# Kernel tuning notes

Hardware: AMD Instinct MI355X
Metric: run time of the kernel (lower is better)

Reference implementation:

```python
import jax, jax.numpy as jnp
import numpy as np

B, S, D = 2, 2048, 2048
NH = 16
HD = D // NH  # 128
MAX_POS = 4096
ROPE_THETA = 10000.0


def rotate_half(x):
    x1, x2 = x[..., : x.shape[-1] // 2], x[..., x.shape[-1] // 2 :]
    return jnp.concatenate((-x2, x1), axis=-1)


def rope_tables(dtype=jnp.float32):
    inv_freq = 1.0 / (ROPE_THETA ** (jnp.arange(0, HD, 2, dtype=jnp.float32) / HD))
    t = jnp.arange(MAX_POS, dtype=jnp.float32)
    freqs = jnp.outer(t, inv_freq)              # [MAX_POS, HD/2]
    emb = jnp.concatenate((freqs, freqs), axis=-1)  # [MAX_POS, HD]
    return jnp.cos(emb).astype(dtype), jnp.sin(emb).astype(dtype)


def setup_inputs() -> dict:
    key = jax.random.key(0)
    ks = jax.random.split(key, 9)
    sc = 0.02
    return {
        "hidden_states": jax.random.normal(ks[0], (B, S, D), jnp.float32),
        "position_ids": jnp.arange(B * S, dtype=jnp.int32).reshape(B, S),
        "Wq": jax.random.normal(ks[1], (D, D), jnp.float32) * sc,
        "bq": jax.random.normal(ks[2], (D,), jnp.float32) * sc,
        "Wk": jax.random.normal(ks[3], (D, D), jnp.float32) * sc,
        "bk": jax.random.normal(ks[4], (D,), jnp.float32) * sc,
        "Wv": jax.random.normal(ks[5], (D, D), jnp.float32) * sc,
        "bv": jax.random.normal(ks[6], (D,), jnp.float32) * sc,
        "Wo": jax.random.normal(ks[7], (D, D), jnp.float32) * sc,
    }


def reference(hidden_states, position_ids, Wq, bq, Wk, bk, Wv, bv, Wo):
    b, s, _ = hidden_states.shape
    # projections (torch Linear: x @ W.T + b)
    q = (hidden_states @ Wq.T + bq).reshape(b, s, NH, HD).transpose(0, 2, 1, 3)
    k = (hidden_states @ Wk.T + bk).reshape(b, s, NH, HD).transpose(0, 2, 1, 3)
    v = (hidden_states @ Wv.T + bv).reshape(b, s, NH, HD).transpose(0, 2, 1, 3)
    # RoPE
    cos_t, sin_t = rope_tables(hidden_states.dtype)
    cos = cos_t[position_ids][:, None, :, :]  # [B,1,S,HD]
    sin = sin_t[position_ids][:, None, :, :]
    q = q * cos + rotate_half(q) * sin
    k = k * cos + rotate_half(k) * sin
    # NOTE: faithful to the source bug — softmax is computed but its result is
    # discarded; the AV matmul uses the UNNORMALIZED scaled scores.
    attn_weights = jnp.einsum("bhqd,bhkd->bhqk", q, k) / (HD ** 0.5)
    _ = jax.nn.softmax(attn_weights.astype(jnp.float32), axis=-1)  # dead, as in source
    attn_output = jnp.einsum("bhqk,bhkd->bhqd", attn_weights, v)
    attn_output = attn_output.transpose(0, 2, 1, 3).reshape(b, s, D)
    return attn_output @ Wo.T
```

## Files before the change

kernel.cpp:

```cpp
#include <hip/hip_runtime.h>
#include <hip/hip_bf16.h>


typedef __attribute__((ext_vector_type(8))) short bf16x8s;
typedef __attribute__((ext_vector_type(4))) float f32x4;

__device__ __forceinline__ ushort f2bf(float f) {
    union { float f; unsigned int u; } x; x.f = f;
    unsigned int u = x.u;
    unsigned int r = (u + 0x7fffu + ((u >> 16) & 1u)) >> 16;
    return (ushort)r;
}
__device__ __forceinline__ float b2f(ushort u) {
    union { unsigned int u; float f; } x; x.u = ((unsigned int)u) << 16;
    return x.f;
}

__device__ __forceinline__ void gload_lds16(const void* g, void* l) {
    __builtin_amdgcn_global_load_lds((__attribute__((address_space(1))) const void*)g,
                                     (__attribute__((address_space(3))) void*)l, 16, 0, 0);
}

template<bool BIAS, bool OBF16>
__global__ __launch_bounds__(512, 2)
void gemm256(const ushort* __restrict__ A, const ushort* __restrict__ B,
             const float* __restrict__ bias, void* __restrict__ Cv,
             int K, int lda, int ldb, int ldc,
             long sAb, long sBb, long sCb)
{
    __shared__ char smem[131072];
    char* ldsA = smem;
    char* ldsB = smem + 65536;

    int z = blockIdx.z;
    const ushort* Ab = A + (size_t)sAb * z;
    const ushort* Bb = B + (size_t)sBb * z;
    size_t Coff = (size_t)sCb * z;

    int nwgx = gridDim.x;
    int nwg = nwgx * gridDim.y;
    int wg = blockIdx.y * nwgx + blockIdx.x;
    int swz = ((nwg & 7) == 0) ? (wg & 7) * (nwg >> 3) + (wg >> 3) : wg;
    int m0 = (swz % nwgx) * 256;
    int n0 = (swz / nwgx) * 256;

    int tid = threadIdx.x;
    int l = tid & 63, wid = tid >> 6;
    int wm = (wid >> 2) * 128;
    int wn = (wid & 3) * 64;
    int lr = l & 15, lj = l >> 4;

    int offA[8], offB[4];
#pragma unroll
    for (int m = 0; m < 8; m++) {
        int r = wm + m * 16 + lr;
        offA[m] = (r >> 1) * 128 + (((((r & 1) << 2) | lj) ^ ((r >> 1) & 7)) << 4);
    }
#pragma unroll
    for (int n = 0; n < 4; n++) {
        int r = wn + n * 16 + lr;
        offB[n] = (r >> 1) * 128 + (((((r & 1) << 2) | lj) ^ ((r >> 1) & 7)) << 4);
    }

    size_t srcA[2], srcB[2];
    int dstOff[2];
#pragma unroll
    for (int s = 0; s < 2; s++) {
        int c = tid + s * 512;
        int pr = c >> 3;
        int up = (c & 7) ^ (pr & 7);
        int r = (pr << 1) | (up >> 2);
        int jj = up & 3;
        srcA[s] = (size_t)(m0 + r) * lda + jj * 8;
        srcB[s] = (size_t)(n0 + r) * ldb + jj * 8;
        dstOff[s] = c * 16;
    }

    f32x4 acc[8][4];
#pragma unroll
    for (int m = 0; m < 8; m++)
#pragma unroll
        for (int n = 0; n < 4; n++)
            acc[m][n] = (f32x4){0.f, 0.f, 0.f, 0.f};

    int NT2 = K >> 5;

#define STAGE256(T) { int _bo = ((T) & 3) * 16384; size_t _ko = (size_t)(T) * 32; \
    gload_lds16(Ab + srcA[0] + _ko, ldsA + _bo + dstOff[0]); \
    gload_lds16(Ab + srcA[1] + _ko, ldsA + _bo + dstOff[1]); \
    gload_lds16(Bb + srcB[0] + _ko, ldsB + _bo + dstOff[0]); \
    gload_lds16(Bb + srcB[1] + _ko, ldsB + _bo + dstOff[1]); }

    STAGE256(0);
    STAGE256(1);
    asm volatile("s_waitcnt vmcnt(4)" ::: "memory");
    __builtin_amdgcn_s_barrier();

    for (int t = 0; t < NT2; ++t) {
        if (t + 2 < NT2) {
            STAGE256(t + 2);
            __builtin_amdgcn_sched_barrier(0);
        }
        int bo = (t & 3) * 16384;
        bf16x8s bf[4];
#pragma unroll
        for (int n = 0; n < 4; n++)
            bf[n] = *(const bf16x8s*)(ldsB + bo + offB[n]);
        bf16x8s af[8];
#pragma unroll
        for (int m = 0; m < 8; m++)
            af[m] = *(const bf16x8s*)(ldsA + bo + offA[m]);
#pragma unroll
        for (int m = 0; m < 8; m++)
#pragma unroll
            for (int n = 0; n < 4; n++)
                acc[m][n] = __builtin_amdgcn_mfma_f32_16x16x32_bf16(
                    af[m], bf[n], acc[m][n], 0, 0, 0);
        if (t + 1 < NT2) {
            if (t + 2 < NT2) asm volatile("s_waitcnt vmcnt(4)" ::: "memory");
            else             asm volatile("s_waitcnt vmcnt(0)" ::: "memory");
            __builtin_amdgcn_s_barrier();
        }
    }
#undef STAGE256

    int rr = lj * 4;
#pragma unroll
    for (int m = 0; m < 8; m++) {
#pragma unroll
        for (int n = 0; n < 4; n++) {
            int gr = m0 + wm + m * 16 + rr;
            int gc = n0 + wn + n * 16 + lr;
            float bv = BIAS ? bias[gc] : 0.f;
#pragma unroll
            for (int r = 0; r < 4; r++) {
                float v = acc[m][n][r] + bv;
                size_t off = Coff + (size_t)(gr + r) * ldc + gc;
                if (OBF16) ((ushort*)Cv)[off] = f2bf(v);
                else       ((float*)Cv)[off]  = v;
            }
        }
    }
}

template<bool BIAS, bool OBF16, int BN>
__global__ __launch_bounds__(256)
void gemm_nt(const ushort* __restrict__ A, const ushort* __restrict__ B,
             const float* __restrict__ bias, void* __restrict__ Cv,
             int K, int lda, int ldb, int ldc, int ZH,
             long sAb, long sAh, long sBb, long sBh, long sCb, long sCh)
{
    __shared__ ushort As[128 * 32];
    __shared__ ushort Bs[BN * 32];

    int z  = blockIdx.z;
    int zb = z / ZH, zh = z - zb * ZH;
    const ushort* Ab = A + (size_t)(sAb * zb + sAh * zh);
    const ushort* Bb = B + (size_t)(sBb * zb + sBh * zh);
    size_t Coff = (size_t)(sCb * zb + sCh * zh);

    int m0 = blockIdx.x * 128, n0 = blockIdx.y * BN;
    int t = threadIdx.x;
    int l = t & 63, w = t >> 6;
    int wm, wn;
    if (BN == 128) { wm = (w >> 1) * 64; wn = (w & 1) * 64; }
    else           { wm = w * 32;        wn = 0; }
    constexpr int FM = (BN == 128) ? 4 : 2;
    constexpr int FN = 4;
    int lr = l & 15, lk = (l >> 4) * 8;

    f32x4 acc[FM][FN];
#pragma unroll
    for (int i = 0; i < FM; i++)
#pragma unroll
        for (int j = 0; j < FN; j++)
            acc[i][j] = (f32x4){0.f, 0.f, 0.f, 0.f};

    int c0 = t, c1 = t + 256;
    int r0 = c0 >> 2, k0c = (c0 & 3) * 8;
    int r1 = c1 >> 2, k1c = (c1 & 3) * 8;

    for (int kt = 0; kt < K; kt += 32) {
        __syncthreads();
        gload_lds16(Ab + (size_t)(m0 + r0) * lda + kt + k0c, &As[c0 * 8]);
        gload_lds16(Ab + (size_t)(m0 + r1) * lda + kt + k1c, &As[c1 * 8]);
        gload_lds16(Bb + (size_t)(n0 + r0) * ldb + kt + k0c, &Bs[c0 * 8]);
        if (BN == 128)
            gload_lds16(Bb + (size_t)(n0 + r1) * ldb + kt + k1c, &Bs[c1 * 8]);
        __syncthreads();

        bf16x8s af[FM], bf[FN];
#pragma unroll
        for (int i = 0; i < FM; i++)
            af[i] = *(const bf16x8s*)&As[(wm + i * 16 + lr) * 32 + lk];
#pragma unroll
        for (int i = 0; i < FN; i++)
            bf[i] = *(const bf16x8s*)&Bs[(wn + i * 16 + lr) * 32 + lk];
#pragma unroll
        for (int mi = 0; mi < FM; mi++)
#pragma unroll
            for (int ni = 0; ni < FN; ni++)
                acc[mi][ni] = __builtin_amdgcn_mfma_f32_16x16x32_bf16(
                    af[mi], bf[ni], acc[mi][ni], 0, 0, 0);
    }

    int rr = (l >> 4) * 4;
#pragma unroll
    for (int mi = 0; mi < FM; mi++) {
#pragma unroll
        for (int ni = 0; ni < FN; ni++) {
            int gr = m0 + wm + mi * 16 + rr;
            int gc = n0 + wn + ni * 16 + lr;
            float bv = BIAS ? bias[gc] : 0.f;
#pragma unroll
            for (int r = 0; r < 4; r++) {
                float v = acc[mi][ni][r] + bv;
                size_t off = Coff + (size_t)(gr + r) * ldc + gc;
                if (OBF16) ((ushort*)Cv)[off] = f2bf(v);
                else       ((float*)Cv)[off]  = v;
            }
        }
    }
}

__global__ __launch_bounds__(256)
void rope_qk(ushort* __restrict__ QKV, const int* __restrict__ pos,
             ushort* __restrict__ QB)
{
    int tid = blockIdx.x * 256 + threadIdx.x;
    int row = tid >> 7;
    int r = tid & 127;
    int h = r >> 3, j = r & 7;
    int d0 = j * 8;
    float p = (float)pos[row];
    size_t qb = (size_t)row * 6144 + h * 128 + d0;

    bf16x8s q1 = *(const bf16x8s*)&QKV[qb];
    bf16x8s q2 = *(const bf16x8s*)&QKV[qb + 64];
    bf16x8s k1 = *(const bf16x8s*)&QKV[qb + 2048];
    bf16x8s k2 = *(const bf16x8s*)&QKV[qb + 2048 + 64];
    bf16x8s oq1, oq2, ok1, ok2;
#pragma unroll
    for (int i = 0; i < 8; i++) {
        float d = (float)(d0 + i);
        float ang = p * exp2f(d * (-13.287712379549449f / 64.0f));
        float s, c;
        sincosf(ang, &s, &c);
        float a = b2f((ushort)q1[i]), b = b2f((ushort)q2[i]);
        oq1[i] = (short)f2bf(a * c - b * s);
        oq2[i] = (short)f2bf(b * c + a * s);
        float e = b2f((ushort)k1[i]), f = b2f((ushort)k2[i]);
        ok1[i] = (short)f2bf(e * c - f * s);
        ok2[i] = (short)f2bf(f * c + e * s);
    }
    size_t ob = (size_t)row * 2048 + h * 128 + d0;
    *(bf16x8s*)&QB[ob]      = oq1;
    *(bf16x8s*)&QB[ob + 64] = oq2;
    *(bf16x8s*)&QKV[qb + 2048]      = ok1;
    *(bf16x8s*)&QKV[qb + 2048 + 64] = ok2;
}

__global__ __launch_bounds__(256)
void ktv_partial(const ushort* __restrict__ QKV, float* __restrict__ part)
{
    int bh = blockIdx.x;
    int b = bh >> 4, h = bh & 15;
    int s0 = blockIdx.y * 128;
    const ushort* Kp = QKV + (size_t)(b * 2048 + s0) * 6144 + 2048 + h * 128;
    const ushort* Vp = Kp + 2048;

    __shared__ ushort Ks[32][128];
    __shared__ ushort Vs[32][128];

    int t = threadIdx.x;
    int tx = t & 15, ty = t >> 4;
    float acc[8][8];
#pragma unroll
    for (int i = 0; i < 8; i++)
#pragma unroll
        for (int j = 0; j < 8; j++) acc[i][j] = 0.f;

    for (int sb = 0; sb < 128; sb += 32) {
        __syncthreads();
#pragma unroll
        for (int i = 0; i < 2; i++) {
            int idx = t + i * 256;
            int rw = idx >> 4, c8 = (idx & 15) * 8;
            *(bf16x8s*)&Ks[rw][c8] = *(const bf16x8s*)&Kp[(size_t)(sb + rw) * 6144 + c8];
            *(bf16x8s*)&Vs[rw][c8] = *(const bf16x8s*)&Vp[(size_t)(sb + rw) * 6144 + c8];
        }
        __syncthreads();
        for (int ss = 0; ss < 32; ss++) {
            bf16x8s kvv = *(const bf16x8s*)&Ks[ss][tx * 8];
            bf16x8s vvv = *(const bf16x8s*)&Vs[ss][ty * 8];
            float kv[8], vv[8];
#pragma unroll
            for (int i = 0; i < 8; i++) { kv[i] = b2f((ushort)kvv[i]); vv[i] = b2f((ushort)vvv[i]); }
#pragma unroll
            for (int i = 0; i < 8; i++)
#pragma unroll
                for (int j = 0; j < 8; j++)
                    acc[i][j] += kv[i] * vv[j];
        }
    }
    float* pp = part + ((size_t)blockIdx.y * 32 + bh) * 16384;
#pragma unroll
    for (int i = 0; i < 8; i++)
#pragma unroll
        for (int j = 0; j < 8; j++)
            pp[(tx * 8 + i) * 128 + (ty * 8 + j)] = acc[i][j];
}

__global__ __launch_bounds__(256)
void reduce_ktv(const float* __restrict__ part, ushort* __restrict__ Mb)
{
    int i = blockIdx.x * 256 + threadIdx.x;
    float s = 0.f;
#pragma unroll
    for (int p = 0; p < 16; p++) s += part[(size_t)p * 524288 + i];
    Mb[i] = f2bf(s * 0.08838834764831845f);
}

__global__ __launch_bounds__(256)
void conv_f32_bf16(const float* __restrict__ in, ushort* __restrict__ out, int n4)
{
    int i = blockIdx.x * 256 + threadIdx.x;
    if (i >= n4) return;
    float4 v = ((const float4*)in)[i];
    ushort4 o;
    o.x = f2bf(v.x); o.y = f2bf(v.y); o.z = f2bf(v.z); o.w = f2bf(v.w);
    ((ushort4*)out)[i] = o;
}

__global__ __launch_bounds__(256)
void conv_weights(const float* __restrict__ w0, const float* __restrict__ w1,
                  const float* __restrict__ w2, const float* __restrict__ w3,
                  ushort* __restrict__ qkv, ushort* __restrict__ wo)
{
    int i = blockIdx.x * 256 + threadIdx.x;
    int id = i >> 20;
    int off = i & 1048575;
    const float* src = (id == 0) ? w0 : (id == 1) ? w1 : (id == 2) ? w2 : w3;
    float4 v = ((const float4*)src)[off];
    ushort4 o;
    o.x = f2bf(v.x); o.y = f2bf(v.y); o.z = f2bf(v.z); o.w = f2bf(v.w);
    if (id < 3) ((ushort4*)qkv)[(size_t)id * 1048576 + off] = o;
    else        ((ushort4*)wo)[off] = o;
}

__global__ __launch_bounds__(256)
void pack_bias(const float* __restrict__ bq, const float* __restrict__ bk,
               const float* __restrict__ bv, float* __restrict__ bqkv)
{
    int i = blockIdx.x * 256 + threadIdx.x;
    float v = (i < 2048) ? bq[i] : (i < 4096) ? bk[i - 2048] : bv[i - 4096];
    bqkv[i] = v;
}

extern "C" void kernel_launch(void* const* d_in, const int* in_sizes, int n_in,
                              void* d_out, int out_size, void* d_ws, size_t ws_size,
                              hipStream_t stream)
{
    const float* hs = (const float*)d_in[0];
    const int*  pos = (const int*)d_in[1];
    const float* Wq = (const float*)d_in[2];
    const float* bq = (const float*)d_in[3];
    const float* Wk = (const float*)d_in[4];
    const float* bk = (const float*)d_in[5];
    const float* Wv = (const float*)d_in[6];
    const float* bv = (const float*)d_in[7];
    const float* Wo = (const float*)d_in[8];
    float* out = (float*)d_out;
    char* ws = (char*)d_ws;

    ushort* HSB  = (ushort*)(ws + 0);
    ushort* QB   = (ushort*)(ws + 0);
    ushort* WQKV = (ushort*)(ws + 16777216);
    ushort* NT   = (ushort*)(ws + 16777216);
    ushort* WOB  = (ushort*)(ws + 41943040);
    float*  BQKV = (float*)(ws + 50331648);
    ushort* QKVB = (ushort*)(ws + 50356224);
    ushort* MB   = (ushort*)(ws + 100687872);
    float*  PART = out;

    dim3 blk(256);

    conv_f32_bf16<<<8192, blk, 0, stream>>>(hs, HSB, 2097152);
    conv_weights<<<16384, blk, 0, stream>>>(Wq, Wk, Wv, Wo, WQKV, WOB);
    pack_bias<<<24, blk, 0, stream>>>(bq, bk, bv, BQKV);

    gemm256<true, true><<<dim3(16, 24, 1), dim3(512), 0, stream>>>(
        HSB, WQKV, BQKV, QKVB, 2048, 2048, 2048, 6144, 0, 0, 0);

    rope_qk<<<2048, blk, 0, stream>>>(QKVB, pos, QB);

    ktv_partial<<<dim3(32, 16, 1), blk, 0, stream>>>(QKVB, PART);
    reduce_ktv<<<2048, blk, 0, stream>>>(PART, MB);

    gemm_nt<false, true, 128><<<dim3(16, 1, 32), blk, 0, stream>>>(
        WOB, MB, nullptr, NT, 128, 2048, 128, 2048, 16,
        0, 128, 262144, 16384, 4194304, 128);

    gemm256<false, false><<<dim3(8, 8, 2), dim3(512), 0, stream>>>(
        QB, NT, nullptr, out, 2048, 2048, 2048, 2048,
        4194304, 4194304, 4194304);
}
```

Before: 393.2 us.

## Restructure GEMM main loop into four-phase ping-pong with interleaved staging

Reworks the 256x256 GEMM mainloop to process 64-wide K tiles in two 64KB LDS halves. Each iteration runs four phases that interleave the A/B prefetch into the other half with half-tile MFMA blocks, separated by barriers and s_setprio. Source offsets drop from 64-bit to 32-bit. The aim is to overlap global-to-LDS loads with MFMA work and cut address-computation registers. In exchange it adds more barriers per K step and needs careful vmcnt accounting.

```diff
diff --git a/kernel.cpp b/kernel.cpp
--- a/kernel.cpp
+++ b/kernel.cpp
@@ -29,8 +29,6 @@
              long sAb, long sBb, long sCb)
 {
     __shared__ char smem[131072];
-    char* ldsA = smem;
-    char* ldsB = smem + 65536;
 
     int z = blockIdx.z;
     const ushort* Ab = A + (size_t)sAb * z;
@@ -62,18 +60,18 @@
         offB[n] = (r >> 1) * 128 + (((((r & 1) << 2) | lj) ^ ((r >> 1) & 7)) << 4);
     }
 
-    size_t srcA[2], srcB[2];
-    int dstOff[2];
-#pragma unroll
-    for (int s = 0; s < 2; s++) {
-        int c = tid + s * 512;
-        int pr = c >> 3;
-        int up = (c & 7) ^ (pr & 7);
-        int r = (pr << 1) | (up >> 2);
-        int jj = up & 3;
-        srcA[s] = (size_t)(m0 + r) * lda + jj * 8;
-        srcB[s] = (size_t)(n0 + r) * ldb + jj * 8;
-        dstOff[s] = c * 16;
+    unsigned srcA0, srcA1, srcB0, srcB1;
+    int dst0 = tid * 16, dst1 = dst0 + 8192;
+    {
+        int c0 = tid, c1 = tid + 512;
+        int pr0 = c0 >> 3, up0 = (c0 & 7) ^ (pr0 & 7);
+        int r0 = (pr0 << 1) | (up0 >> 2), j0 = up0 & 3;
+        int pr1 = c1 >> 3, up1 = (c1 & 7) ^ (pr1 & 7);
+        int r1 = (pr1 << 1) | (up1 >> 2), j1 = up1 & 3;
+        srcA0 = (unsigned)(m0 + r0) * lda + j0 * 8;
+        srcA1 = (unsigned)(m0 + r1) * lda + j1 * 8;
+        srcB0 = (unsigned)(n0 + r0) * ldb + j0 * 8;
+        srcB1 = (unsigned)(n0 + r1) * ldb + j1 * 8;
     }
 
     f32x4 acc[8][4];
@@ -83,46 +81,82 @@
         for (int n = 0; n < 4; n++)
             acc[m][n] = (f32x4){0.f, 0.f, 0.f, 0.f};
 
-    int NT2 = K >> 5;
-
-#define STAGE256(T) { int _bo = ((T) & 3) * 16384; size_t _ko = (size_t)(T) * 32; \
-    gload_lds16(Ab + srcA[0] + _ko, ldsA + _bo + dstOff[0]); \
-    gload_lds16(Ab + srcA[1] + _ko, ldsA + _bo + dstOff[1]); \
-    gload_lds16(Bb + srcB[0] + _ko, ldsB + _bo + dstOff[0]); \
-    gload_lds16(Bb + srcB[1] + _ko, ldsB + _bo + dstOff[1]); }
-
-    STAGE256(0);
-    STAGE256(1);
+    int NT = K >> 6;
+
+#define STAGE_A(ldsbyte, eoff) { \
+    gload_lds16(Ab + srcA0 + (eoff), smem + (ldsbyte) + dst0); \
+    gload_lds16(Ab + srcA1 + (eoff), smem + (ldsbyte) + dst1); }
+#define STAGE_B(ldsbyte, eoff) { \
+    gload_lds16(Bb + srcB0 + (eoff), smem + (ldsbyte) + dst0); \
+    gload_lds16(Bb + srcB1 + (eoff), smem + (ldsbyte) + dst1); }
+#define LDA_FRAGS(mb, kadd) { \
+    _Pragma("unroll") \
+    for (int m = 0; m < 4; m++) \
+        af[m] = *(const bf16x8s*)(smem + lb + offA[(mb) + m] + (kadd)); }
+#define LDB_FRAGS(kadd) { \
+    _Pragma("unroll") \
+    for (int n = 0; n < 4; n++) \
+        bf[n] = *(const bf16x8s*)(smem + lb + 32768 + offB[n] + (kadd)); }
+#define DO_MFMA(mb) { \
+    __builtin_amdgcn_s_setprio(1); \
+    _Pragma("unroll") \
+    for (int m = 0; m < 4; m++) \
+        _Pragma("unroll") \
+        for (int n = 0; n < 4; n++) \
+            acc[(mb) + m][n] = __builtin_amdgcn_mfma_f32_16x16x32_bf16( \
+                af[m], bf[n], acc[(mb) + m][n], 0, 0, 0); \
+    __builtin_amdgcn_s_setprio(0); }
+#define ENTER_PHASE() { __builtin_amdgcn_s_barrier(); \
+    asm volatile("s_waitcnt lgkmcnt(0)" ::: "memory"); \
+    __builtin_amdgcn_sched_barrier(0); }
+
+    STAGE_A(0, 0);
+    STAGE_B(32768, 0);
+    STAGE_A(16384, 32);
+    STAGE_B(49152, 32);
     asm volatile("s_waitcnt vmcnt(4)" ::: "memory");
     __builtin_amdgcn_s_barrier();
 
-    for (int t = 0; t < NT2; ++t) {
-        if (t + 2 < NT2) {
-            STAGE256(t + 2);
-            __builtin_amdgcn_sched_barrier(0);
-        }
-        int bo = (t & 3) * 16384;
-        bf16x8s bf[4];
-#pragma unroll
-        for (int n = 0; n < 4; n++)
-            bf[n] = *(const bf16x8s*)(ldsB + bo + offB[n]);
-        bf16x8s af[8];
-#pragma unroll
-        for (int m = 0; m < 8; m++)
-            af[m] = *(const bf16x8s*)(ldsA + bo + offA[m]);
-#pragma unroll
-        for (int m = 0; m < 8; m++)
-#pragma unroll
-            for (int n = 0; n < 4; n++)
-                acc[m][n] = __builtin_amdgcn_mfma_f32_16x16x32_bf16(
-                    af[m], bf[n], acc[m][n], 0, 0, 0);
-        if (t + 1 < NT2) {
-            if (t + 2 < NT2) asm volatile("s_waitcnt vmcnt(4)" ::: "memory");
-            else             asm volatile("s_waitcnt vmcnt(0)" ::: "memory");
-            __builtin_amdgcn_s_barrier();
-        }
-    }
-#undef STAGE256
+    for (int t = 0; t < NT; ++t) {
+        int lb = (t & 1) << 16;
+        int pb = lb ^ 65536;
+        bool pf = (t + 1 < NT);
+        unsigned eo = (unsigned)(t + 1) * 64;
+        bf16x8s af[4], bf[4];
+
+        LDA_FRAGS(0, 0); LDB_FRAGS(0);
+        if (pf) STAGE_A(pb, eo);
+        ENTER_PHASE();
+        DO_MFMA(0);
+        __builtin_amdgcn_s_barrier();
+
+        LDA_FRAGS(4, 0);
+        if (pf) STAGE_B(pb + 32768, eo);
+        ENTER_PHASE();
+        DO_MFMA(4);
+        if (pf) asm volatile("s_waitcnt vmcnt(4)" ::: "memory");
+        else    asm volatile("s_waitcnt vmcnt(0)" ::: "memory");
+        __builtin_amdgcn_s_barrier();
+
+        LDA_FRAGS(0, 16384); LDB_FRAGS(16384);
+        if (pf) STAGE_A(pb + 16384, eo + 32);
+        ENTER_PHASE();
+        DO_MFMA(0);
+        __builtin_amdgcn_s_barrier();
+
+        LDA_FRAGS(4, 16384);
+        if (pf) STAGE_B(pb + 49152, eo + 32);
+        ENTER_PHASE();
+        DO_MFMA(4);
+        if (pf) asm volatile("s_waitcnt vmcnt(4)" ::: "memory");
+        __builtin_amdgcn_s_barrier();
+    }
+#undef STAGE_A
+#undef STAGE_B
+#undef LDA_FRAGS
+#undef LDB_FRAGS
+#undef DO_MFMA
+#undef ENTER_PHASE
 
     int rr = lj * 4;
 #pragma unroll
```

New measurement: 393.3 us. No clear change (+0.0%).
